# Kernel tuning notes

Hardware: AMD Instinct MI355X
Metric: run time of the kernel (lower is better)

## Reference

```python
import jax, jax.numpy as jnp
import numpy as np
from jax import lax

B, L, D_MODEL = 4, 1024, 512
D_STATE, D_CONV, D_INNER = 16, 4, 2 * D_MODEL


def setup_inputs() -> dict:
    key = jax.random.key(0)
    ks = jax.random.split(key, 8)
    s = 0.02
    x = jax.random.normal(ks[0], (B, L, D_MODEL), dtype=jnp.float32)
    W_in = jax.random.normal(ks[1], (D_MODEL, 2 * D_INNER), dtype=jnp.float32) * s
    conv_w = jax.random.normal(ks[2], (D_INNER, 1, D_CONV), dtype=jnp.float32) * s  # OIH, depthwise
    conv_b = jnp.zeros((D_INNER,), jnp.float32)
    W_x = jax.random.normal(ks[3], (D_INNER, 2 * D_STATE), dtype=jnp.float32) * s
    W_dt = jax.random.normal(ks[4], (D_INNER, D_INNER), dtype=jnp.float32) * s
    b_dt = jnp.zeros((D_INNER,), jnp.float32)
    # A_log = -logspace(log10(0.001), log10(1.0), d_state); used directly as A in the scan
    A_log = -jnp.logspace(np.log10(1e-3), 0.0, D_STATE, dtype=jnp.float32)
    D_skip = jnp.ones((D_INNER,), jnp.float32) * 0.1
    W_out = jax.random.normal(ks[5], (D_INNER, D_MODEL), dtype=jnp.float32) * s
    gamma = jnp.ones((D_MODEL,), jnp.float32)
    beta = jnp.zeros((D_MODEL,), jnp.float32)
    return dict(x=x, W_in=W_in, conv_w=conv_w, conv_b=conv_b, W_x=W_x, W_dt=W_dt,
                b_dt=b_dt, A_log=A_log, D_skip=D_skip, W_out=W_out, gamma=gamma, beta=beta)


def _mamba_forward(x, W_in, conv_w, conv_b, W_x, W_dt, b_dt, A_log, D_skip, W_out, gamma, beta):
    x = jnp.clip(x, -10.0, 10.0)
    x_and_res = x @ W_in                                  # [B, L, 2*d_inner]
    xp, res = jnp.split(x_and_res, 2, axis=-1)
    # Depthwise causal conv1d: torch pads d_conv-1 both sides then slices [:L] -> left-pad only.
    xt = jnp.transpose(xp, (0, 2, 1))                     # [B, d_inner, L]
    xc = lax.conv_general_dilated(xt, conv_w, window_strides=(1,),
                                  padding=[(D_CONV - 1, 0)],
                                  dimension_numbers=('NCH', 'OIH', 'NCH'),
                                  feature_group_count=D_INNER)
    xc = xc + conv_b[None, :, None]
    xc = jax.nn.silu(jnp.transpose(xc, (0, 2, 1)))        # [B, L, d_inner]
    ssm = xc @ W_x                                        # [B, L, 2*d_state]
    Bm, Cm = jnp.split(ssm, 2, axis=-1)                   # each [B, L, d_state]
    delta = xc @ W_dt + b_dt                              # [B, L, d_inner] (no softplus in source)

    # Selective scan over time (sequential recurrence)
    def step(h, inp):
        u_t, d_t, B_t, C_t = inp                          # [B,I], [B,I], [B,S], [B,S]
        dA = jnp.exp(jnp.clip(d_t[:, :, None] * A_log, -5.0, 5.0))   # [B, I, S]
        h = dA * h + (d_t[:, :, None] * B_t[:, None, :]) * u_t[:, :, None]
        y = jnp.einsum('bis,bs->bi', h, C_t)
        return h, y

    tm = lambda a: jnp.swapaxes(a, 0, 1)                  # time-major
    h0 = jnp.zeros((x.shape[0], D_INNER, D_STATE), xc.dtype)
    _, ys = lax.scan(step, h0, (tm(xc), tm(delta), tm(Bm), tm(Cm)))
    y = jnp.swapaxes(ys, 0, 1) + xc * D_skip              # D skip connection

    y = y * jax.nn.silu(res)                              # gating
    out = y @ W_out
    r = out + x                                           # residual
    mu = jnp.mean(r, axis=-1, keepdims=True)
    var = jnp.var(r, axis=-1, keepdims=True)
    return gamma * (r - mu) / jnp.sqrt(var + 1e-5) + beta


def reference(x, W_in, conv_w, conv_b, W_x, W_dt, b_dt, A_log, D_skip, W_out, gamma, beta):
    return _mamba_forward(x, W_in, conv_w, conv_b, W_x, W_dt, b_dt, A_log, D_skip, W_out, gamma, beta)
```

## Files before the change

kernel.cpp:

```cpp
#include <hip/hip_runtime.h>
#include <hip/hip_bf16.h>

typedef __hip_bfloat16 bf16;
typedef unsigned short ushort_t;
typedef unsigned int uint_t;
typedef __attribute__((ext_vector_type(8))) __bf16 bf16x8;
typedef __attribute__((ext_vector_type(4))) float f32x4;

#define BB 4
#define LL 1024
#define DM 512
#define DS 16
#define DI 1024
#define ROWS 4096
#define NC 64
#define CT 16
#define NDTX 1152

__device__ __forceinline__ float b2f(bf16 v) { return __bfloat162float(v); }

__device__ __forceinline__ float load_flag(const void* src, int i, int isbf)
{
    return isbf ? b2f(((const bf16*)src)[i]) : ((const float*)src)[i];
}

__device__ __forceinline__ ushort_t f2b_bits(float v)
{
    bf16 t = __float2bfloat16(v);
    return *(ushort_t*)&t;
}

__device__ __forceinline__ float bits2f(ushort_t u)
{
    uint_t w = ((uint_t)u) << 16;
    return __uint_as_float(w);
}

__device__ __forceinline__ int detect_local(const ushort_t* wdt)
{
    __shared__ int bad;
    if (threadIdx.x == 0) bad = 0;
    __syncthreads();
    ushort_t u = wdt[threadIdx.x & 255];
    if (((u >> 7) & 0xFF) >= 127) atomicAdd(&bad, 1);
    __syncthreads();
    return (bad <= 8) ? 1 : 0;
}

__global__ __launch_bounds__(256)
void prep_all(const void* x, const void* Win, const void* Wdt, const void* Wx,
              const void* Wout, const void* cw, const void* cb, const void* Alog,
              const void* Dsk, const void* gam, const void* bet, const void* bdt,
              bf16* __restrict__ xbf, bf16* __restrict__ WtIn,
              bf16* __restrict__ WtDtx, bf16* __restrict__ WtOut,
              float* __restrict__ ccw, float* __restrict__ ccb,
              float* __restrict__ cAlg, float* __restrict__ cDsk,
              float* __restrict__ cgam, float* __restrict__ cbet,
              float* __restrict__ bdtx)
{
    const int isbf = detect_local((const ushort_t*)Wdt);
    int blk = blockIdx.x;

    if (blk < 2048) {
        int idx = blk * 256 + threadIdx.x;
        float v[4];
        if (isbf) {
            uint2 raw = ((const uint2*)x)[idx];
            v[0] = __uint_as_float(raw.x << 16);
            v[1] = __uint_as_float(raw.x & 0xFFFF0000u);
            v[2] = __uint_as_float(raw.y << 16);
            v[3] = __uint_as_float(raw.y & 0xFFFF0000u);
        } else {
            float4 raw = ((const float4*)x)[idx];
            v[0] = raw.x; v[1] = raw.y; v[2] = raw.z; v[3] = raw.w;
        }
        uint_t b0, b1;
        b0 = f2b_bits(fminf(fmaxf(v[0], -10.f), 10.f))
           | ((uint_t)f2b_bits(fminf(fmaxf(v[1], -10.f), 10.f)) << 16);
        b1 = f2b_bits(fminf(fmaxf(v[2], -10.f), 10.f))
           | ((uint_t)f2b_bits(fminf(fmaxf(v[3], -10.f), 10.f)) << 16);
        uint2 ow; ow.x = b0; ow.y = b1;
        ((uint2*)xbf)[idx] = ow;
    } else if (blk < 4640) {
        int tb = blk - 2048;
        const void* src; bf16* dst; int K, Nsrc, tpr;
        if (tb < 1024)      { src = Win;  dst = WtIn;               K = 512;  Nsrc = 2048; tpr = 64; }
        else if (tb < 2048) { tb -= 1024; src = Wdt;  dst = WtDtx;  K = 1024; Nsrc = 1024; tpr = 32; }
        else if (tb < 2080) { tb -= 2048; src = Wx;   dst = WtDtx + 1024 * 1024; K = 1024; Nsrc = 32; tpr = 1; }
        else                { tb -= 2080; src = Wout; dst = WtOut;  K = 1024; Nsrc = 512;  tpr = 16; }
        int k0 = (tb / tpr) * 32, n0 = (tb % tpr) * 32;

        __shared__ float tile[32][33];
        int tx = threadIdx.x & 31, ty = threadIdx.x >> 5;
        #pragma unroll
        for (int j = 0; j < 4; ++j)
            tile[ty + 8 * j][tx] = load_flag(src, (k0 + ty + 8 * j) * Nsrc + n0 + tx, isbf);
        __syncthreads();
        #pragma unroll
        for (int j = 0; j < 4; ++j)
            dst[(size_t)(n0 + ty + 8 * j) * K + k0 + tx] = __float2bfloat16(tile[tx][ty + 8 * j]);
    } else {
        int i = (blk - 4640) * 256 + threadIdx.x;
        if (i < 4096)        ccw[i] = load_flag(cw, i, isbf);
        else if (i < 5120)   ccb[i - 4096] = load_flag(cb, i - 4096, isbf);
        else if (i < 5136)   cAlg[i - 5120] = load_flag(Alog, i - 5120, isbf);
        else if (i < 6160)   cDsk[i - 5136] = load_flag(Dsk, i - 5136, isbf);
        else if (i < 6672)   cgam[i - 6160] = load_flag(gam, i - 6160, isbf);
        else if (i < 7184)   cbet[i - 6672] = load_flag(bet, i - 6672, isbf);
        else if (i < 8336) {
            int j = i - 7184;
            bdtx[j] = (j < DI) ? load_flag(bdt, j, isbf) : 0.f;
        } else if (i < 106640) {
            (WtDtx + 1056 * 1024)[i - 8336] = __float2bfloat16(0.f);
        }
    }
}

__device__ __forceinline__ void gload16(const bf16* g, ushort_t* l)
{
    __builtin_amdgcn_global_load_lds(
        (const __attribute__((address_space(1))) void*)g,
        (__attribute__((address_space(3))) void*)l, 16, 0, 0);
}

template <int TM, int TN, bool OBF>
__global__ __launch_bounds__(256)
void gemm_mfma(const bf16* __restrict__ A, const bf16* __restrict__ Bt,
               const float* __restrict__ bias, void* __restrict__ Cv,
               int M, int N, int K)
{
    constexpr int MI = TM / 32, NJ = TN / 32;
    constexpr int NQA = TM * 8 / 256;
    constexpr int NQB = TN * 8 / 256;
    __shared__ ushort_t As[TM * 64];
    __shared__ ushort_t Bs[TN * 64];

    const int tid = threadIdx.x;
    const int lane = tid & 63;
    const int w = tid >> 6;
    const int wr = w >> 1, wc = w & 1;
    const int m0 = blockIdx.y * TM;
    const int n0 = blockIdx.x * TN;

    const bf16* gA[NQA]; ushort_t* lA[NQA];
    #pragma unroll
    for (int q = 0; q < NQA; ++q) {
        int p = q * 256 + tid;
        int row = p >> 3, kc = ((p & 7) - row) & 7;
        gA[q] = A + (size_t)(m0 + row) * K + kc * 8;
        lA[q] = &As[(q * 256 + w * 64) * 8];
    }
    const bf16* gB[NQB]; ushort_t* lB[NQB];
    #pragma unroll
    for (int q = 0; q < NQB; ++q) {
        int p = q * 256 + tid;
        int row = p >> 3, kc = ((p & 7) - row) & 7;
        gB[q] = Bt + (size_t)(n0 + row) * K + kc * 8;
        lB[q] = &Bs[(q * 256 + w * 64) * 8];
    }

    f32x4 acc[MI][NJ];
    #pragma unroll
    for (int i = 0; i < MI; ++i)
        #pragma unroll
        for (int j = 0; j < NJ; ++j)
            acc[i][j] = (f32x4){0.f, 0.f, 0.f, 0.f};

    const int ko = lane >> 4;
    const int ml = lane & 15;

    for (int k0 = 0; k0 < K; k0 += 64) {
        #pragma unroll
        for (int q = 0; q < NQA; ++q) gload16(gA[q] + k0, lA[q]);
        #pragma unroll
        for (int q = 0; q < NQB; ++q) gload16(gB[q] + k0, lB[q]);
        __syncthreads();

        #pragma unroll
        for (int half = 0; half < 2; ++half) {
            bf16x8 af[MI], bfr[NJ];
            #pragma unroll
            for (int i = 0; i < MI; ++i) {
                int m = wr * (TM / 2) + i * 16 + ml;
                af[i] = *(const bf16x8*)&As[(m * 8 + ((half * 4 + ko + m) & 7)) * 8];
            }
            #pragma unroll
            for (int j = 0; j < NJ; ++j) {
                int n = wc * (TN / 2) + j * 16 + ml;
                bfr[j] = *(const bf16x8*)&Bs[(n * 8 + ((half * 4 + ko + n) & 7)) * 8];
            }
            #pragma unroll
            for (int i = 0; i < MI; ++i)
                #pragma unroll
                for (int j = 0; j < NJ; ++j)
                    acc[i][j] = __builtin_amdgcn_mfma_f32_16x16x32_bf16(
                        af[i], bfr[j], acc[i][j], 0, 0, 0);
        }
        __syncthreads();
    }

    const int rq = lane >> 4;
    #pragma unroll
    for (int j = 0; j < NJ; ++j) {
        int n = n0 + wc * (TN / 2) + j * 16 + ml;
        float bv = bias ? bias[n] : 0.f;
        #pragma unroll
        for (int i = 0; i < MI; ++i) {
            int mb = m0 + wr * (TM / 2) + i * 16 + rq * 4;
            #pragma unroll
            for (int r = 0; r < 4; ++r) {
                float v = acc[i][j][r] + bv;
                if (OBF) ((bf16*)Cv)[(size_t)(mb + r) * N + n] = __float2bfloat16(v);
                else     ((float*)Cv)[(size_t)(mb + r) * N + n] = v;
            }
        }
    }
}

__global__ __launch_bounds__(256)
void conv_silu(const bf16* __restrict__ xrb, const float* __restrict__ cw,
               const float* __restrict__ cb, bf16* __restrict__ xcb)
{
    int idx = blockIdx.x * 256 + threadIdx.x;
    int i = idx & (DI - 1);
    int row = idx >> 10;
    int t = row & (LL - 1);

    float w0 = cw[i * 4 + 0];
    float w1 = cw[i * 4 + 1];
    float w2 = cw[i * 4 + 2];
    float w3 = cw[i * 4 + 3];

    float acc = cb[i];
    const bf16* base = xrb + (size_t)row * 2048 + i;
    if (t >= 3) acc = fmaf(b2f(base[-3 * 2048]), w0, acc);
    if (t >= 2) acc = fmaf(b2f(base[-2 * 2048]), w1, acc);
    if (t >= 1) acc = fmaf(b2f(base[-1 * 2048]), w2, acc);
    acc = fmaf(b2f(base[0]), w3, acc);

    xcb[idx] = __float2bfloat16(acc / (1.f + __expf(-acc)));
}

__global__ __launch_bounds__(1024)
void scan_fused(const bf16* __restrict__ xcb, const bf16* __restrict__ dlx,
                const bf16* __restrict__ xrb, const float* __restrict__ A_log,
                const float* __restrict__ Dskip, bf16* __restrict__ ybf)
{
    __shared__ ushort_t lp[NC * 16 * DS];
    __shared__ ushort_t lq[NC * 16 * DS];

    const int b = blockIdx.x >> 6;
    const int ch0 = (blockIdx.x & 63) << 4;
    const int chl = threadIdx.x & 15;
    const int c = threadIdx.x >> 4;
    const int i = ch0 + chl;

    float a[DS];
    #pragma unroll
    for (int s = 0; s < DS; ++s) a[s] = A_log[s];

    const int row0 = b * LL + c * CT;
    float d[CT], u[CT];
    float h[DS] = {};
    float p[DS];
    #pragma unroll
    for (int s = 0; s < DS; ++s) p[s] = 1.f;

    for (int t = 0; t < CT; ++t) {
        const size_t row = row0 + t;
        d[t] = b2f(dlx[row * NDTX + i]);
        u[t] = b2f(xcb[row * DI + i]);
        const bf16* sp = dlx + row * NDTX + 1024;
        #pragma unroll
        for (int s = 0; s < DS; ++s) {
            float e = fminf(fmaxf(d[t] * a[s], -5.f), 5.f);
            float dA = __expf(e);
            h[s] = fmaf(dA, h[s], (d[t] * b2f(sp[s])) * u[t]);
            p[s] *= dA;
        }
    }
    {
        const int off = (c * 16 + chl) * DS;
        #pragma unroll
        for (int s = 0; s < DS; ++s) {
            lp[off + s] = f2b_bits(p[s]);
            lq[off + s] = f2b_bits(h[s]);
        }
    }
    __syncthreads();

    if (threadIdx.x < 256) {
        int cl = threadIdx.x & 15;
        int s = threadIdx.x >> 4;
        float hh = 0.f;
        for (int cc = 0; cc < NC; ++cc) {
            int off = (cc * 16 + cl) * DS + s;
            float pp = bits2f(lp[off]);
            float qq = bits2f(lq[off]);
            lp[off] = f2b_bits(hh);
            hh = fmaf(pp, hh, qq);
        }
    }
    __syncthreads();

    {
        const int off = (c * 16 + chl) * DS;
        #pragma unroll
        for (int s = 0; s < DS; ++s) h[s] = bits2f(lp[off + s]);
    }
    const float dsk = Dskip[i];
    for (int t = 0; t < CT; ++t) {
        const size_t row = row0 + t;
        const bf16* sp = dlx + row * NDTX + 1024;
        float y = 0.f;
        #pragma unroll
        for (int s = 0; s < DS; ++s) {
            float e = fminf(fmaxf(d[t] * a[s], -5.f), 5.f);
            float dA = __expf(e);
            h[s] = fmaf(dA, h[s], (d[t] * b2f(sp[s])) * u[t]);
            y = fmaf(h[s], b2f(sp[DS + s]), y);
        }
        float res = b2f(xrb[row * 2048 + DI + i]);
        float g = res / (1.f + __expf(-res));
        ybf[row * DI + i] = __float2bfloat16((y + u[t] * dsk) * g);
    }
}

__global__ __launch_bounds__(256)
void ln_kernel(const float* __restrict__ outp, const void* __restrict__ xsrc,
               const void* __restrict__ wdt_probe,
               const float* __restrict__ gamma, const float* __restrict__ beta,
               void* __restrict__ out)
{
    const int isbf = detect_local((const ushort_t*)wdt_probe);
    const int row = blockIdx.x;
    const int tid = threadIdx.x;

    float r[2];
    float sum = 0.f, ss = 0.f;
    #pragma unroll
    for (int q = 0; q < 2; ++q) {
        int j = tid + q * 256;
        float xv = load_flag(xsrc, row * DM + j, isbf);
        xv = fminf(fmaxf(xv, -10.f), 10.f);
        float v = outp[(size_t)row * DM + j] + xv;
        r[q] = v;
        sum += v;
        ss = fmaf(v, v, ss);
    }
    #pragma unroll
    for (int off = 32; off >= 1; off >>= 1) {
        sum += __shfl_down(sum, off);
        ss  += __shfl_down(ss, off);
    }
    __shared__ float s1[4], s2[4];
    __shared__ float stats[2];
    int wid = tid >> 6, lane = tid & 63;
    if (lane == 0) { s1[wid] = sum; s2[wid] = ss; }
    __syncthreads();
    if (tid == 0) {
        float S = s1[0] + s1[1] + s1[2] + s1[3];
        float Qq = s2[0] + s2[1] + s2[2] + s2[3];
        float mean = S / DM;
        float var = Qq / DM - mean * mean;
        stats[0] = mean;
        stats[1] = rsqrtf(var + 1e-5f);
    }
    __syncthreads();
    float mean = stats[0], rstd = stats[1];
    #pragma unroll
    for (int q = 0; q < 2; ++q) {
        int j = tid + q * 256;
        float v = (r[q] - mean) * rstd * gamma[j] + beta[j];
        size_t o = (size_t)row * DM + j;
        if (isbf) ((bf16*)out)[o] = __float2bfloat16(v);
        else      ((float*)out)[o] = v;
    }
}

extern "C" void kernel_launch(void* const* d_in, const int* in_sizes, int n_in,
                              void* d_out, int out_size, void* d_ws, size_t ws_size,
                              hipStream_t stream)
{
    float* W = (float*)d_ws;
    float* ccw  = W;
    float* ccb  = ccw  + 4096;
    float* cAlg = ccb  + 1024;
    float* cDsk = cAlg + 16;
    float* cgam = cDsk + 1024;
    float* cbet = cgam + 512;
    float* bdtx = cbet + 512;
    float* outp = bdtx + 1152;
    bf16*  xbf  = (bf16*)(outp + 2097152);
    bf16*  xrb  = xbf  + 2097152;
    bf16*  xcb  = xrb  + 8388608;
    bf16*  ybf  = xcb  + 4194304;
    bf16*  dlx  = ybf  + 4194304;
    bf16*  WtIn = dlx  + 4718592;
    bf16*  WtDtx= WtIn + 1048576;
    bf16*  WtOut= WtDtx+ 1179648;

    prep_all<<<5057, 256, 0, stream>>>(
        d_in[0], d_in[1], d_in[5], d_in[4], d_in[9], d_in[2], d_in[3],
        d_in[7], d_in[8], d_in[10], d_in[11], d_in[6],
        xbf, WtIn, WtDtx, WtOut, ccw, ccb, cAlg, cDsk, cgam, cbet, bdtx);

    gemm_mfma<64, 128, true><<<dim3(2048 / 128, ROWS / 64), 256, 0, stream>>>(
        xbf, WtIn, nullptr, xrb, ROWS, 2048, 512);

    conv_silu<<<ROWS * DI / 256, 256, 0, stream>>>(xrb, ccw, ccb, xcb);

    gemm_mfma<64, 128, true><<<dim3(NDTX / 128, ROWS / 64), 256, 0, stream>>>(
        xcb, WtDtx, bdtx, dlx, ROWS, NDTX, DI);

    scan_fused<<<256, 1024, 0, stream>>>(xcb, dlx, xrb, cAlg, cDsk, ybf);

    gemm_mfma<64, 64, false><<<dim3(DM / 64, ROWS / 64), 256, 0, stream>>>(
        ybf, WtOut, nullptr, outp, ROWS, DM, DI);

    ln_kernel<<<ROWS, 256, 0, stream>>>(outp, d_in[0], d_in[5], cgam, cbet, d_out);
}
```

Before: 226.4 us.

## Vectorize conv_silu and restructure scan shared-memory layout and B/C loads

conv_silu now processes 8 channels per thread with 16-byte vector loads and stores, cutting the thread count by 8x and the number of scalar memory transactions. In scan_fused, the per-chunk P and H summaries are packed into one 32-bit LDS word in an s-major layout, which should avoid bank conflicts in the sequential chunk-combine pass. B and C are read as 8-wide vectors instead of scalar bf16 loads. d and u are no longer kept in register arrays and are reloaded in the second pass, trading some extra global reads for lower register pressure.

```diff
diff --git a/kernel.cpp b/kernel.cpp
--- a/kernel.cpp
+++ b/kernel.cpp
@@ -5,6 +5,7 @@
 typedef unsigned short ushort_t;
 typedef unsigned int uint_t;
 typedef __attribute__((ext_vector_type(8))) __bf16 bf16x8;
+typedef __attribute__((ext_vector_type(8))) ushort_t u16x8;
 typedef __attribute__((ext_vector_type(4))) float f32x4;
 
 #define BB 4
@@ -222,23 +223,29 @@
                const float* __restrict__ cb, bf16* __restrict__ xcb)
 {
     int idx = blockIdx.x * 256 + threadIdx.x;
-    int i = idx & (DI - 1);
-    int row = idx >> 10;
+    int i = (idx & 127) * 8;
+    int row = idx >> 7;
     int t = row & (LL - 1);
 
-    float w0 = cw[i * 4 + 0];
-    float w1 = cw[i * 4 + 1];
-    float w2 = cw[i * 4 + 2];
-    float w3 = cw[i * 4 + 3];
-
-    float acc = cb[i];
-    const bf16* base = xrb + (size_t)row * 2048 + i;
-    if (t >= 3) acc = fmaf(b2f(base[-3 * 2048]), w0, acc);
-    if (t >= 2) acc = fmaf(b2f(base[-2 * 2048]), w1, acc);
-    if (t >= 1) acc = fmaf(b2f(base[-1 * 2048]), w2, acc);
-    acc = fmaf(b2f(base[0]), w3, acc);
-
-    xcb[idx] = __float2bfloat16(acc / (1.f + __expf(-acc)));
+    const u16x8 zv = {0, 0, 0, 0, 0, 0, 0, 0};
+    const ushort_t* base = (const ushort_t*)(xrb) + (size_t)row * 2048 + i;
+    u16x8 r3 = *(const u16x8*)base;
+    u16x8 r2 = (t >= 1) ? *(const u16x8*)(base - 2048) : zv;
+    u16x8 r1 = (t >= 2) ? *(const u16x8*)(base - 4096) : zv;
+    u16x8 r0 = (t >= 3) ? *(const u16x8*)(base - 6144) : zv;
+
+    u16x8 out;
+    #pragma unroll
+    for (int k = 0; k < 8; ++k) {
+        float4 w = ((const float4*)cw)[i + k];
+        float acc = cb[i + k];
+        acc = fmaf(bits2f(r0[k]), w.x, acc);
+        acc = fmaf(bits2f(r1[k]), w.y, acc);
+        acc = fmaf(bits2f(r2[k]), w.z, acc);
+        acc = fmaf(bits2f(r3[k]), w.w, acc);
+        out[k] = f2b_bits(acc / (1.f + __expf(-acc)));
+    }
+    *(u16x8*)((ushort_t*)xcb + (size_t)row * DI + i) = out;
 }
 
 __global__ __launch_bounds__(1024)
@@ -246,13 +253,13 @@
                 const bf16* __restrict__ xrb, const float* __restrict__ A_log,
                 const float* __restrict__ Dskip, bf16* __restrict__ ybf)
 {
-    __shared__ ushort_t lp[NC * 16 * DS];
-    __shared__ ushort_t lq[NC * 16 * DS];
-
+    __shared__ uint_t lsum[DS * NC * 16];
+
+    const int tid = threadIdx.x;
     const int b = blockIdx.x >> 6;
     const int ch0 = (blockIdx.x & 63) << 4;
-    const int chl = threadIdx.x & 15;
-    const int c = threadIdx.x >> 4;
+    const int chl = tid & 15;
+    const int c = tid >> 4;
     const int i = ch0 + chl;
 
     float a[DS];
@@ -260,7 +267,6 @@
     for (int s = 0; s < DS; ++s) a[s] = A_log[s];
 
     const int row0 = b * LL + c * CT;
-    float d[CT], u[CT];
     float h[DS] = {};
     float p[DS];
     #pragma unroll
@@ -268,61 +274,63 @@
 
     for (int t = 0; t < CT; ++t) {
         const size_t row = row0 + t;
-        d[t] = b2f(dlx[row * NDTX + i]);
-        u[t] = b2f(xcb[row * DI + i]);
-        const bf16* sp = dlx + row * NDTX + 1024;
+        float d = bits2f(((const ushort_t*)dlx)[row * NDTX + i]);
+        float u = bits2f(((const ushort_t*)xcb)[row * DI + i]);
+        float du = d * u;
+        const u16x8* sp = (const u16x8*)(dlx + row * NDTX + 1024);
+        u16x8 B0 = sp[0], B1 = sp[1];
         #pragma unroll
         for (int s = 0; s < DS; ++s) {
-            float e = fminf(fmaxf(d[t] * a[s], -5.f), 5.f);
+            float e = fminf(fmaxf(d * a[s], -5.f), 5.f);
             float dA = __expf(e);
-            h[s] = fmaf(dA, h[s], (d[t] * b2f(sp[s])) * u[t]);
+            float Bv = bits2f(s < 8 ? B0[s] : B1[s - 8]);
+            h[s] = fmaf(dA, h[s], du * Bv);
             p[s] *= dA;
         }
     }
-    {
-        const int off = (c * 16 + chl) * DS;
-        #pragma unroll
-        for (int s = 0; s < DS; ++s) {
-            lp[off + s] = f2b_bits(p[s]);
-            lq[off + s] = f2b_bits(h[s]);
-        }
-    }
-    __syncthreads();
-
-    if (threadIdx.x < 256) {
-        int cl = threadIdx.x & 15;
-        int s = threadIdx.x >> 4;
+    #pragma unroll
+    for (int s = 0; s < DS; ++s)
+        lsum[s * 1024 + tid] = (uint_t)f2b_bits(p[s]) | ((uint_t)f2b_bits(h[s]) << 16);
+    __syncthreads();
+
+    if (tid < 256) {
+        int cl = tid & 15, s = tid >> 4;
         float hh = 0.f;
         for (int cc = 0; cc < NC; ++cc) {
-            int off = (cc * 16 + cl) * DS + s;
-            float pp = bits2f(lp[off]);
-            float qq = bits2f(lq[off]);
-            lp[off] = f2b_bits(hh);
+            int off = s * 1024 + cc * 16 + cl;
+            uint_t wrd = lsum[off];
+            float pp = bits2f((ushort_t)(wrd & 0xFFFF));
+            float qq = bits2f((ushort_t)(wrd >> 16));
+            lsum[off] = (uint_t)f2b_bits(hh);
             hh = fmaf(pp, hh, qq);
         }
     }
     __syncthreads();
 
-    {
-        const int off = (c * 16 + chl) * DS;
-        #pragma unroll
-        for (int s = 0; s < DS; ++s) h[s] = bits2f(lp[off + s]);
-    }
+    #pragma unroll
+    for (int s = 0; s < DS; ++s) h[s] = bits2f((ushort_t)lsum[s * 1024 + tid]);
+
     const float dsk = Dskip[i];
     for (int t = 0; t < CT; ++t) {
         const size_t row = row0 + t;
-        const bf16* sp = dlx + row * NDTX + 1024;
+        float d = bits2f(((const ushort_t*)dlx)[row * NDTX + i]);
+        float u = bits2f(((const ushort_t*)xcb)[row * DI + i]);
+        float du = d * u;
+        const u16x8* sp = (const u16x8*)(dlx + row * NDTX + 1024);
+        u16x8 B0 = sp[0], B1 = sp[1], C0 = sp[2], C1 = sp[3];
         float y = 0.f;
         #pragma unroll
         for (int s = 0; s < DS; ++s) {
-            float e = fminf(fmaxf(d[t] * a[s], -5.f), 5.f);
+            float e = fminf(fmaxf(d * a[s], -5.f), 5.f);
             float dA = __expf(e);
-            h[s] = fmaf(dA, h[s], (d[t] * b2f(sp[s])) * u[t]);
-            y = fmaf(h[s], b2f(sp[DS + s]), y);
-        }
-        float res = b2f(xrb[row * 2048 + DI + i]);
+            float Bv = bits2f(s < 8 ? B0[s] : B1[s - 8]);
+            float Cv = bits2f(s < 8 ? C0[s] : C1[s - 8]);
+            h[s] = fmaf(dA, h[s], du * Bv);
+            y = fmaf(h[s], Cv, y);
+        }
+        float res = bits2f(((const ushort_t*)xrb)[row * 2048 + DI + i]);
         float g = res / (1.f + __expf(-res));
-        ybf[row * DI + i] = __float2bfloat16((y + u[t] * dsk) * g);
+        ybf[row * DI + i] = __float2bfloat16((y + u * dsk) * g);
     }
 }
 
@@ -408,7 +416,7 @@
     gemm_mfma<64, 128, true><<<dim3(2048 / 128, ROWS / 64), 256, 0, stream>>>(
         xbf, WtIn, nullptr, xrb, ROWS, 2048, 512);
 
-    conv_silu<<<ROWS * DI / 256, 256, 0, stream>>>(xrb, ccw, ccb, xcb);
+    conv_silu<<<ROWS * DI / 8 / 256, 256, 0, stream>>>(xrb, ccw, ccb, xcb);
 
     gemm_mfma<64, 128, true><<<dim3(NDTX / 128, ROWS / 64), 256, 0, stream>>>(
         xcb, WtDtx, bdtx, dlx, ROWS, NDTX, DI);
```

Result: faster. 218.0 us (-3.7%).
